# Performance work log

Measured on AMD Instinct MI355X. Metric: run time of the kernel, lower is better.

Reference implementation:

```python
import jax, jax.numpy as jnp
import numpy as np
from jax import lax

B = 16
IMG = 384
P = 16
C = 3
DIM = 256
DEPTH = 6
HEADS = 4
DH = 64
INNER = HEADS * DH  # 256
MLP = 512
NC = 21
HP = IMG // P       # 24
N = HP * HP         # 576
PD = C * P * P      # 768
K = 16
SCALE = DH ** -0.5
NEG = -1e9


def _ln(x, g, b):
    mu = x.mean(-1, keepdims=True)
    var = ((x - mu) ** 2).mean(-1, keepdims=True)
    return (x - mu) / jnp.sqrt(var + 1e-5) * g + b


def _conv(x, w, b):
    y = lax.conv_general_dilated(x, w, (1, 1), 'SAME',
                                 dimension_numbers=('NCHW', 'OIHW', 'NCHW'))
    return y + b[None, :, None, None]


def _up2(x):
    b, c, h, w = x.shape
    return jax.image.resize(x, (b, c, 2 * h, 2 * w), 'bilinear')


def _attn(x, g, bt, qkv_w, out_w, out_b, alpha):
    xn = _ln(x, g, bt)
    qkv = xn @ qkv_w                              # [B,N,3*INNER]
    q, k, v = jnp.split(qkv, 3, axis=-1)
    def heads(t):
        return t.reshape(B, N, HEADS, DH).transpose(0, 2, 1, 3)  # b h n d
    q, k, v = heads(q), heads(k), heads(v)
    dots = jnp.einsum('bhid,bhjd->bhij', q, k) * SCALE           # [B,H,N,N]
    vals, idx = lax.top_k(dots, K)                               # [B,H,N,K]
    bi = jnp.arange(B)[:, None, None, None]
    hi = jnp.arange(HEADS)[None, :, None, None]
    ni = jnp.arange(N)[None, None, :, None]
    sparse = jnp.full(dots.shape, NEG, dots.dtype).at[bi, hi, ni, idx].set(vals)
    sparse_attn = jax.nn.softmax(sparse, axis=-1)
    global_attn = jax.nn.softmax(dots, axis=-1)
    a = jnp.clip(alpha, 0.0, 1.0)
    attn = (1 - a) * sparse_attn + a * global_attn
    out = jnp.einsum('bhij,bhjd->bhid', attn, v)                 # [B,H,N,DH]
    out = out.transpose(0, 2, 1, 3).reshape(B, N, INNER)
    return out @ out_w + out_b


def _forward(img, patch_w, patch_b, pos_emb,
             ln1_g, ln1_b, qkv_w, out_w, out_b, alpha,
             ln2_g, ln2_b, ff_w1, ff_b1, ff_w2, ff_b2,
             lnf_g, lnf_b,
             conv1_w, conv1_b, conv2_w, conv2_b, conv3_w, conv3_b):
    # patchify: b c (h p1) (w p2) -> b (h w) (p1 p2 c)
    x = img.reshape(B, C, HP, P, HP, P).transpose(0, 2, 4, 3, 5, 1).reshape(B, N, PD)
    x = x @ patch_w + patch_b + pos_emb
    for i in range(DEPTH):
        x = x + _attn(x, ln1_g[i], ln1_b[i], qkv_w[i], out_w[i], out_b[i], alpha[i])
        h = _ln(x, ln2_g[i], ln2_b[i])
        h = jax.nn.gelu(h @ ff_w1[i] + ff_b1[i], approximate=False)
        x = x + h @ ff_w2[i] + ff_b2[i]
    x = _ln(x, lnf_g, lnf_b)
    x = x.transpose(0, 2, 1).reshape(B, DIM, HP, HP)             # b d h w
    x = jax.nn.relu(_conv(x, conv1_w, conv1_b))
    x = _up2(x)
    x = jax.nn.relu(_conv(x, conv2_w, conv2_b))
    x = _up2(x)
    x = _conv(x, conv3_w, conv3_b)
    return jax.image.resize(x, (B, NC, IMG, IMG), 'bilinear')


def setup_inputs() -> dict:
    key = jax.random.key(0)
    ks = jax.random.split(key, 16)
    s = 0.02
    d = {
        'img': jax.random.normal(ks[0], (B, C, IMG, IMG), jnp.float32),
        'patch_w': jax.random.normal(ks[1], (PD, DIM)) * s,
        'patch_b': jnp.zeros((DIM,)),
        'pos_emb': jax.random.normal(ks[2], (1, N, DIM)) * s,
        'ln1_g': jnp.ones((DEPTH, DIM)), 'ln1_b': jnp.zeros((DEPTH, DIM)),
        'qkv_w': jax.random.normal(ks[3], (DEPTH, DIM, 3 * INNER)) * s,
        'out_w': jax.random.normal(ks[4], (DEPTH, INNER, DIM)) * s,
        'out_b': jnp.zeros((DEPTH, DIM)),
        'alpha': jnp.full((DEPTH,), 0.2),
        'ln2_g': jnp.ones((DEPTH, DIM)), 'ln2_b': jnp.zeros((DEPTH, DIM)),
        'ff_w1': jax.random.normal(ks[5], (DEPTH, DIM, MLP)) * s,
        'ff_b1': jnp.zeros((DEPTH, MLP)),
        'ff_w2': jax.random.normal(ks[6], (DEPTH, MLP, DIM)) * s,
        'ff_b2': jnp.zeros((DEPTH, DIM)),
        'lnf_g': jnp.ones((DIM,)), 'lnf_b': jnp.zeros((DIM,)),
        'conv1_w': jax.random.normal(ks[7], (DIM // 2, DIM, 3, 3)) * s,
        'conv1_b': jnp.zeros((DIM // 2,)),
        'conv2_w': jax.random.normal(ks[8], (DIM // 4, DIM // 2, 3, 3)) * s,
        'conv2_b': jnp.zeros((DIM // 4,)),
        'conv3_w': jax.random.normal(ks[9], (NC, DIM // 4, 1, 1)) * s,
        'conv3_b': jnp.zeros((NC,)),
    }
    return d


def reference(img, patch_w, patch_b, pos_emb,
              ln1_g, ln1_b, qkv_w, out_w, out_b, alpha,
              ln2_g, ln2_b, ff_w1, ff_b1, ff_w2, ff_b2,
              lnf_g, lnf_b,
              conv1_w, conv1_b, conv2_w, conv2_b, conv3_w, conv3_b):
    return _forward(img, patch_w, patch_b, pos_emb,
                    ln1_g, ln1_b, qkv_w, out_w, out_b, alpha,
                    ln2_g, ln2_b, ff_w1, ff_b1, ff_w2, ff_b2,
                    lnf_g, lnf_b,
                    conv1_w, conv1_b, conv2_w, conv2_b, conv3_w, conv3_b)
```

## Files before the change

### kernel.cpp

```cpp
#include <hip/hip_runtime.h>
#include <cfloat>
#include <cmath>

constexpr int NB    = 16;
constexpr int IMGSZ = 384;
constexpr int PSZ   = 16;
constexpr int NCH   = 3;
constexpr int DMODEL= 256;
constexpr int DEPTH = 6;
constexpr int NHEAD = 4;
constexpr int DHEAD = 64;
constexpr int DQKV  = 768;
constexpr int QKS   = 512;
constexpr int DMLP  = 512;
constexpr int NCLS  = 21;
constexpr int HPATCH= 24;
constexpr int NTOK  = 576;
constexpr int NPD   = 768;
constexpr int TOPK  = 16;
constexpr int NROWS = NB * NTOK;
constexpr int OUT_TOTAL = NB * NCLS * IMGSZ * IMGSZ;

constexpr int RPB    = 16;
constexpr int NBLK   = NTOK / RPB;
constexpr int CHUNK  = 64;
constexpr int NCHUNK = NTOK / CHUNK;
constexpr int SCP    = 577;

typedef __attribute__((ext_vector_type(8))) short bf16x8;
typedef __attribute__((ext_vector_type(4))) float f32x4;

__device__ __forceinline__ unsigned short f2bf(float f) {
    unsigned u = __builtin_bit_cast(unsigned, f);
    unsigned r = (u + 0x7FFFu + ((u >> 16) & 1u)) >> 16;
    return (unsigned short)r;
}
__device__ __forceinline__ float bf2f(unsigned short h) {
    unsigned u = ((unsigned)h) << 16;
    return __builtin_bit_cast(float, u);
}

__global__ __launch_bounds__(256) void k_castT(const float* __restrict__ src,
                                               unsigned short* __restrict__ dst,
                                               int K, int N) {
    int t = blockIdx.x * 256 + threadIdx.x;
    if (t >= K * N) return;
    size_t base = (size_t)blockIdx.y * K * N;
    int n = t / K, k = t - n * K;
    dst[base + t] = f2bf(src[base + (size_t)k * N + n]);
}

template <int IC>
__global__ __launch_bounds__(256) void k_castConv(const float* __restrict__ src,
                                                  unsigned short* __restrict__ dst,
                                                  int OC) {
    int t = blockIdx.x * 256 + threadIdx.x;
    if (t >= OC * 9 * IC) return;
    int oc = t / (9 * IC);
    int r = t - oc * 9 * IC;
    int tap = r / IC, ic = r - tap * IC;
    dst[t] = f2bf(src[((size_t)(oc * IC + ic)) * 9 + tap]);
}

__global__ __launch_bounds__(256) void k_patchify(const float* __restrict__ img,
                                                  unsigned short* __restrict__ A) {
    int t = blockIdx.x * 256 + threadIdx.x;
    if (t >= NROWS * NPD) return;
    int r  = t / NPD, pd = t - r * NPD;
    int b  = r / NTOK, n = r - b * NTOK;
    int hy = n / HPATCH, hx = n - hy * HPATCH;
    int c  = pd % NCH;  int q = pd / NCH;
    int p2 = q % PSZ;   int p1 = q / PSZ;
    A[t] = f2bf(img[(((size_t)(b * NCH + c)) * IMGSZ + hy * PSZ + p1) * IMGSZ + hx * PSZ + p2]);
}

template <int BM, int BN, int EPI, int CIN>
__global__ __launch_bounds__(256) void k_mm(
    const unsigned short* __restrict__ Abf,
    const unsigned short* __restrict__ Wt,
    const float* __restrict__ bias,
    float* __restrict__ outf,
    unsigned short* __restrict__ outb,
    unsigned short* __restrict__ outb2,
    unsigned short* __restrict__ vth,
    unsigned short* __restrict__ vtl,
    int M, int Nn, int K, int H, int Wd, int gxd, int gyd)
{
    constexpr int MF = BM / 32;
    constexpr int NF = BN / 32;
    constexpr bool GATHER = (CIN > 0);
    constexpr int AREP = BM * 4 / 256;
    constexpr int BREP = BN * 4 / 256;
    __shared__ __align__(16) short As[4][BM][8];
    __shared__ __align__(16) short Bs[4][BN][8];
    const int tid = threadIdx.x;
    const int p = blockIdx.x;
    const int xr = p & 7, xq = p >> 3;
    const int bm = (xr * (gyd >> 3) + xq / gxd) * BM;
    const int bn = (xq % gxd) * BN;
    const int lane = tid & 63, wid = tid >> 6;
    const int wm = wid >> 1, wn = wid & 1;
    const int l15 = lane & 15, lg = lane >> 4;

    int pb_[AREP], py_[AREP], px_[AREP];
    if (GATHER) {
        #pragma unroll
        for (int rep = 0; rep < AREP; ++rep) {
            int idx = rep * 256 + tid;
            int m = idx >> 2;
            int pix = bm + m;
            px_[rep] = pix % Wd;
            int r = pix / Wd;
            py_[rep] = r % H;
            pb_[rep] = r / H;
        }
    }

    f32x4 acc[MF][NF];
    #pragma unroll
    for (int i = 0; i < MF; ++i)
        #pragma unroll
        for (int j = 0; j < NF; ++j)
            acc[i][j] = (f32x4){0.f, 0.f, 0.f, 0.f};

    for (int k0 = 0; k0 < K; k0 += 32) {
        #pragma unroll
        for (int rep = 0; rep < AREP; ++rep) {
            int idx = rep * 256 + tid;
            int m = idx >> 2, kg = idx & 3;
            if (!GATHER) {
                *(bf16x8*)As[kg][m] =
                    *(const bf16x8*)(Abf + (size_t)(bm + m) * K + k0 + kg * 8);
            } else {
                int k = k0 + kg * 8;
                int tap = k / CIN;
                int ic = k - tap * CIN;
                int dy = tap / 3 - 1, dx = tap % 3 - 1;
                int yy = py_[rep] + dy, xx = px_[rep] + dx;
                bf16x8 v = (bf16x8){0, 0, 0, 0, 0, 0, 0, 0};
                if ((unsigned)yy < (unsigned)H && (unsigned)xx < (unsigned)Wd)
                    v = *(const bf16x8*)(Abf +
                        ((size_t)((pb_[rep] * H + yy) * Wd + xx)) * CIN + ic);
                *(bf16x8*)As[kg][m] = v;
            }
        }
        #pragma unroll
        for (int rep = 0; rep < BREP; ++rep) {
            int idx = rep * 256 + tid;
            int n = idx >> 2, kg = idx & 3;
            *(bf16x8*)Bs[kg][n] =
                *(const bf16x8*)(Wt + (size_t)(bn + n) * K + k0 + kg * 8);
        }
        __syncthreads();
        bf16x8 af[MF], bfv[NF];
        #pragma unroll
        for (int i = 0; i < MF; ++i)
            af[i] = *(const bf16x8*)As[lg][wm * (BM / 2) + i * 16 + l15];
        #pragma unroll
        for (int j = 0; j < NF; ++j)
            bfv[j] = *(const bf16x8*)Bs[lg][wn * (BN / 2) + j * 16 + l15];
        #pragma unroll
        for (int i = 0; i < MF; ++i)
            #pragma unroll
            for (int j = 0; j < NF; ++j)
                acc[i][j] = __builtin_amdgcn_mfma_f32_16x16x32_bf16(
                    af[i], bfv[j], acc[i][j], 0, 0, 0);
        __syncthreads();
    }

    if constexpr (EPI == 8) {
        #pragma unroll
        for (int i = 0; i < MF; ++i) {
            const int row0 = bm + wm * (BM / 2) + i * 16 + lg * 4;
            #pragma unroll
            for (int j = 0; j < NF; ++j) {
                const int col = bn + wn * (BN / 2) + j * 16 + l15;
                if (col < 512) {
                    #pragma unroll
                    for (int r = 0; r < 4; ++r) {
                        float v = acc[i][j][r];
                        unsigned short hi = f2bf(v);
                        outb[(size_t)(row0 + r) * QKS + col] = hi;
                        outb2[(size_t)(row0 + r) * QKS + col] = f2bf(v - bf2f(hi));
                    }
                } else {
                    const int d = col - 512, hh = d >> 6, dd = d & 63;
                    const int bb = row0 / NTOK, n = row0 % NTOK;
                    unsigned long long ph = 0ull, pl = 0ull;
                    #pragma unroll
                    for (int r = 0; r < 4; ++r) {
                        float v = acc[i][j][r];
                        unsigned short hi = f2bf(v);
                        unsigned short lo = f2bf(v - bf2f(hi));
                        ph |= (unsigned long long)hi << (16 * r);
                        pl |= (unsigned long long)lo << (16 * r);
                    }
                    const size_t off = (size_t)((bb * NHEAD + hh) * DHEAD + dd) * NTOK + n;
                    *(unsigned long long*)(vth + off) = ph;
                    *(unsigned long long*)(vtl + off) = pl;
                }
            }
        }
    } else {
        #pragma unroll
        for (int i = 0; i < MF; ++i) {
            const int row0 = bm + wm * (BM / 2) + i * 16 + lg * 4;
            #pragma unroll
            for (int j = 0; j < NF; ++j) {
                const int col = bn + wn * (BN / 2) + j * 16 + l15;
                #pragma unroll
                for (int r = 0; r < 4; ++r) {
                    const int rr = row0 + r;
                    float v = acc[i][j][r] + bias[col];
                    if (EPI == 2) v = 0.5f * v * (1.0f + erff(v * 0.70710678118f));
                    if (EPI == 4) v = fmaxf(v, 0.f);
                    outb[(size_t)rr * Nn + col] = f2bf(v);
                }
            }
        }
    }
}

template <int RES>
__global__ __launch_bounds__(256) void k_gemm_ln(
    const unsigned short* __restrict__ Abf,
    const unsigned short* __restrict__ Wt,
    const float* __restrict__ bias,
    const float* __restrict__ extra,
    const float* __restrict__ lng,
    const float* __restrict__ lnb,
    float* __restrict__ x,
    unsigned short* __restrict__ xn,
    int K, int gyd)
{
    constexpr int BM = 32;
    __shared__ __align__(16) short As[4][BM][8];
    __shared__ __align__(16) short Bs[4][256][8];
    __shared__ float redS[BM][4];
    __shared__ float redQ[BM][4];
    const int tid = threadIdx.x;
    const int p = blockIdx.x;
    const int xr = p & 7, xq = p >> 3;
    const int bm = (xr * (gyd >> 3) + xq) * BM;
    const int lane = tid & 63, wn = tid >> 6;
    const int l15 = lane & 15, lg = lane >> 4;

    f32x4 acc[2][4];
    #pragma unroll
    for (int i = 0; i < 2; ++i)
        #pragma unroll
        for (int j = 0; j < 4; ++j)
            acc[i][j] = (f32x4){0.f, 0.f, 0.f, 0.f};

    for (int k0 = 0; k0 < K; k0 += 32) {
        if (tid < BM * 4) {
            int m = tid >> 2, kg = tid & 3;
            *(bf16x8*)As[kg][m] = *(const bf16x8*)(Abf + (size_t)(bm + m) * K + k0 + kg * 8);
        }
        #pragma unroll
        for (int rep = 0; rep < 4; ++rep) {
            int idx = rep * 256 + tid;
            int n = idx >> 2, kg = idx & 3;
            *(bf16x8*)Bs[kg][n] = *(const bf16x8*)(Wt + (size_t)n * K + k0 + kg * 8);
        }
        __syncthreads();
        bf16x8 af[2], bfv[4];
        #pragma unroll
        for (int i = 0; i < 2; ++i)
            af[i] = *(const bf16x8*)As[lg][i * 16 + l15];
        #pragma unroll
        for (int j = 0; j < 4; ++j)
            bfv[j] = *(const bf16x8*)Bs[lg][wn * 64 + j * 16 + l15];
        #pragma unroll
        for (int i = 0; i < 2; ++i)
            #pragma unroll
            for (int j = 0; j < 4; ++j)
                acc[i][j] = __builtin_amdgcn_mfma_f32_16x16x32_bf16(
                    af[i], bfv[j], acc[i][j], 0, 0, 0);
        __syncthreads();
    }

    #pragma unroll
    for (int i = 0; i < 2; ++i) {
        #pragma unroll
        for (int j = 0; j < 4; ++j) {
            const int col = wn * 64 + j * 16 + l15;
            #pragma unroll
            for (int r = 0; r < 4; ++r) {
                const int rr = bm + i * 16 + lg * 4 + r;
                float v = acc[i][j][r] + bias[col];
                if (RES) v += x[(size_t)rr * DMODEL + col];
                else     v += extra[(size_t)(rr % NTOK) * DMODEL + col];
                x[(size_t)rr * DMODEL + col] = v;
                acc[i][j][r] = v;
            }
        }
    }
    float s[2][4];
    #pragma unroll
    for (int i = 0; i < 2; ++i)
        #pragma unroll
        for (int r = 0; r < 4; ++r)
            s[i][r] = ((acc[i][0][r] + acc[i][1][r]) + acc[i][2][r]) + acc[i][3][r];
    #pragma unroll
    for (int off = 1; off < 16; off <<= 1)
        #pragma unroll
        for (int i = 0; i < 2; ++i)
            #pragma unroll
            for (int r = 0; r < 4; ++r)
                s[i][r] += __shfl_xor(s[i][r], off);
    if (l15 == 0)
        #pragma unroll
        for (int i = 0; i < 2; ++i)
            #pragma unroll
            for (int r = 0; r < 4; ++r)
                redS[i * 16 + lg * 4 + r][wn] = s[i][r];
    __syncthreads();
    float mu[2][4];
    #pragma unroll
    for (int i = 0; i < 2; ++i)
        #pragma unroll
        for (int r = 0; r < 4; ++r) {
            const float* q = redS[i * 16 + lg * 4 + r];
            mu[i][r] = (((q[0] + q[1]) + q[2]) + q[3]) * (1.0f / DMODEL);
        }
    float qq[2][4];
    #pragma unroll
    for (int i = 0; i < 2; ++i)
        #pragma unroll
        for (int r = 0; r < 4; ++r) {
            float d0 = acc[i][0][r] - mu[i][r], d1 = acc[i][1][r] - mu[i][r];
            float d2 = acc[i][2][r] - mu[i][r], d3 = acc[i][3][r] - mu[i][r];
            qq[i][r] = ((d0 * d0 + d1 * d1) + d2 * d2) + d3 * d3;
        }
    #pragma unroll
    for (int off = 1; off < 16; off <<= 1)
        #pragma unroll
        for (int i = 0; i < 2; ++i)
            #pragma unroll
            for (int r = 0; r < 4; ++r)
                qq[i][r] += __shfl_xor(qq[i][r], off);
    if (l15 == 0)
        #pragma unroll
        for (int i = 0; i < 2; ++i)
            #pragma unroll
            for (int r = 0; r < 4; ++r)
                redQ[i * 16 + lg * 4 + r][wn] = qq[i][r];
    __syncthreads();
    #pragma unroll
    for (int i = 0; i < 2; ++i) {
        #pragma unroll
        for (int r = 0; r < 4; ++r) {
            const float* q = redQ[i * 16 + lg * 4 + r];
            float var = (((q[0] + q[1]) + q[2]) + q[3]) * (1.0f / DMODEL);
            float rstd = rsqrtf(var + 1e-5f);
            const int rr = bm + i * 16 + lg * 4 + r;
            #pragma unroll
            for (int j = 0; j < 4; ++j) {
                const int col = wn * 64 + j * 16 + l15;
                float o = (acc[i][j][r] - mu[i][r]) * rstd * lng[col] + lnb[col];
                xn[(size_t)rr * DMODEL + col] = f2bf(o);
            }
        }
    }
}

struct KF { bf16x8 h0, h1, l0, l1; };
__device__ __forceinline__ KF ldkf(const unsigned short* __restrict__ hi,
                                   const unsigned short* __restrict__ lo,
                                   size_t off) {
    KF f;
    f.h0 = *(const bf16x8*)(hi + off);
    f.h1 = *(const bf16x8*)(hi + off + 32);
    f.l0 = *(const bf16x8*)(lo + off);
    f.l1 = *(const bf16x8*)(lo + off + 32);
    return f;
}

__global__ __launch_bounds__(512, 8) void k_attn(
    const unsigned short* __restrict__ qhi,
    const unsigned short* __restrict__ qlo,
    const unsigned short* __restrict__ vthi,
    const unsigned short* __restrict__ vtlo,
    const float* __restrict__ alpha_l,
    unsigned short* __restrict__ ao) {
    __shared__ __align__(16) unsigned char ub[16 * SCP * 4];
    float* scp = (float*)ub;
    short* pj  = (short*)ub;
    float* red = (float*)(ub + 16384);

    const int tid = threadIdx.x;
    const int lane = tid & 63;
    const int w = tid >> 6;
    const int par = w >> 2;
    const int ct = w & 3;
    const int l15 = lane & 15, lg = lane >> 4;
    const int xr = blockIdx.x & 7, xq = blockIdx.x >> 3;
    const int g = xr + 8 * (xq / NBLK);
    const int b = g >> 2, h = g & 3;
    const int i0 = (xq % NBLK) * RPB;

    bf16x8 aqh0, aqh1, aql0, aql1;
    {
        const size_t qoff = (size_t)(b * NTOK + i0 + l15) * QKS + h * DHEAD + lg * 8;
        aqh0 = *(const bf16x8*)(qhi + qoff);
        aqh1 = *(const bf16x8*)(qhi + qoff + 32);
        aql0 = *(const bf16x8*)(qlo + qoff);
        aql1 = *(const bf16x8*)(qlo + qoff + 32);
    }

    const size_t kRow = (size_t)(b * NTOK + ct * 16 + l15) * QKS + DMODEL + h * DHEAD + lg * 8;
    for (int c = par; c < NCHUNK; c += 2) {
        KF kc = ldkf(qhi, qlo, kRow + (size_t)c * CHUNK * QKS);
        f32x4 sD = (f32x4){0.f, 0.f, 0.f, 0.f};
        sD = __builtin_amdgcn_mfma_f32_16x16x32_bf16(aqh0, kc.h0, sD, 0, 0, 0);
        sD = __builtin_amdgcn_mfma_f32_16x16x32_bf16(aqh0, kc.l0, sD, 0, 0, 0);
        sD = __builtin_amdgcn_mfma_f32_16x16x32_bf16(aql0, kc.h0, sD, 0, 0, 0);
        sD = __builtin_amdgcn_mfma_f32_16x16x32_bf16(aqh1, kc.h1, sD, 0, 0, 0);
        sD = __builtin_amdgcn_mfma_f32_16x16x32_bf16(aqh1, kc.l1, sD, 0, 0, 0);
        sD = __builtin_amdgcn_mfma_f32_16x16x32_bf16(aql1, kc.h1, sD, 0, 0, 0);
        const int col = c * CHUNK + ct * 16 + l15;
        #pragma unroll
        for (int r = 0; r < 4; ++r)
            scp[(lg * 4 + r) * SCP + col] = sD[r] * 0.125f;
    }
    __syncthreads();

    float o_[2][9];
    const int r0 = 2 * w;
    #pragma unroll
    for (int rr = 0; rr < 2; ++rr)
        #pragma unroll
        for (int t = 0; t < 9; ++t)
            o_[rr][t] = scp[(r0 + rr) * SCP + t * 64 + lane];
    __syncthreads();

    unsigned msk[2] = {0u, 0u};
    float M_[2];
    for (int k = 0; k < TOPK; ++k) {
        float lm[2];
        #pragma unroll
        for (int rr = 0; rr < 2; ++rr) {
            float m0 = -FLT_MAX;
            #pragma unroll
            for (int t = 0; t < 9; ++t) {
                float v = ((msk[rr] >> t) & 1u) ? -FLT_MAX : o_[rr][t];
                m0 = fmaxf(m0, v);
            }
            lm[rr] = m0;
        }
        #pragma unroll
        for (int off = 1; off < 64; off <<= 1) {
            #pragma unroll
            for (int rr = 0; rr < 2; ++rr)
                lm[rr] = fmaxf(lm[rr], __shfl_xor(lm[rr], off));
        }
        if (k == 0) {
            #pragma unroll
            for (int rr = 0; rr < 2; ++rr) M_[rr] = lm[rr];
        }
        #pragma unroll
        for (int rr = 0; rr < 2; ++rr) {
            int js = -1;
            #pragma unroll
            for (int t = 0; t < 9; ++t) {
                if (js < 0) {
                    unsigned long long bal =
                        __ballot((((msk[rr] >> t) & 1u) == 0u) && (o_[rr][t] == lm[rr]));
                    if (bal) js = t * 64 + (int)__builtin_ctzll(bal);
                }
            }
            if ((js & 63) == lane) msk[rr] |= 1u << (js >> 6);
        }
    }

    const float al = fminf(fmaxf(alpha_l[0], 0.f), 1.f);
    float gs[2], ss[2];
    #pragma unroll
    for (int rr = 0; rr < 2; ++rr) {
        float g_ = 0.f, s_ = 0.f;
        #pragma unroll
        for (int t = 0; t < 9; ++t) {
            float e = __expf(o_[rr][t] - M_[rr]);
            g_ += e;
            if ((msk[rr] >> t) & 1u) s_ += e;
        }
        gs[rr] = g_; ss[rr] = s_;
    }
    #pragma unroll
    for (int off = 1; off < 64; off <<= 1) {
        #pragma unroll
        for (int rr = 0; rr < 2; ++rr) {
            gs[rr] += __shfl_xor(gs[rr], off);
            ss[rr] += __shfl_xor(ss[rr], off);
        }
    }
    float ca[2], cs[2];
    #pragma unroll
    for (int rr = 0; rr < 2; ++rr) {
        ca[rr] = al / gs[rr];
        cs[rr] = (1.f - al) / ss[rr];
    }

    const size_t vRow = (size_t)((b * NHEAD + h) * DHEAD + ct * 16 + l15) * NTOK + lg * 8;
    f32x4 acc = (f32x4){0.f, 0.f, 0.f, 0.f};
    for (int c = 0; c < NCHUNK; ++c) {
        short* pb = pj + (c & 1) * (2 * 16 * 72);
        #pragma unroll
        for (int rr = 0; rr < 2; ++rr) {
            float e = __expf(o_[rr][c] - M_[rr]);
            float wv = e * (ca[rr] + (((msk[rr] >> c) & 1u) ? cs[rr] : 0.f));
            unsigned short hi = f2bf(wv);
            pb[(r0 + rr) * 72 + lane] = (short)hi;
            pb[16 * 72 + (r0 + rr) * 72 + lane] = (short)f2bf(wv - bf2f(hi));
        }
        __syncthreads();
        if ((c & 1) == par) {
            KF vc = ldkf(vthi, vtlo, vRow + (size_t)c * CHUNK);
            const short* pr = pb + l15 * 72 + lg * 8;
            bf16x8 ah0 = *(const bf16x8*)(pr);
            bf16x8 ah1 = *(const bf16x8*)(pr + 32);
            bf16x8 al0 = *(const bf16x8*)(pr + 16 * 72);
            bf16x8 al1 = *(const bf16x8*)(pr + 16 * 72 + 32);
            acc = __builtin_amdgcn_mfma_f32_16x16x32_bf16(ah0, vc.h0, acc, 0, 0, 0);
            acc = __builtin_amdgcn_mfma_f32_16x16x32_bf16(ah0, vc.l0, acc, 0, 0, 0);
            acc = __builtin_amdgcn_mfma_f32_16x16x32_bf16(al0, vc.h0, acc, 0, 0, 0);
            acc = __builtin_amdgcn_mfma_f32_16x16x32_bf16(ah1, vc.h1, acc, 0, 0, 0);
            acc = __builtin_amdgcn_mfma_f32_16x16x32_bf16(ah1, vc.l1, acc, 0, 0, 0);
            acc = __builtin_amdgcn_mfma_f32_16x16x32_bf16(al1, vc.h1, acc, 0, 0, 0);
        }
    }
    if (par == 1) {
        #pragma unroll
        for (int r = 0; r < 4; ++r)
            red[(ct * 16 + l15) * 17 + lg * 4 + r] = acc[r];
    }
    __syncthreads();
    if (par == 0) {
        const int qrow = i0 + lg * 4;
        const int dcol = h * DHEAD + ct * 16 + l15;
        #pragma unroll
        for (int r = 0; r < 4; ++r) {
            float v = acc[r] + red[(ct * 16 + l15) * 17 + lg * 4 + r];
            ao[(size_t)(b * NTOK + qrow + r) * DMODEL + dcol] = f2bf(v);
        }
    }
}

__device__ __forceinline__ void bilin_axis(float sF, int H, int& i0, int& i1, float& f) {
    float fl = floorf(sF);
    f = sF - fl;
    int lo = (int)fl;
    i0 = lo < 0 ? 0 : (lo > H - 1 ? H - 1 : lo);
    int hi = lo + 1;
    i1 = hi < 0 ? 0 : (hi > H - 1 ? H - 1 : hi);
}

__global__ __launch_bounds__(256) void k_up2n(const unsigned short* __restrict__ in,
                                              unsigned short* __restrict__ outp,
                                              int Hin, int C) {
    const int Ho = 2 * Hin;
    const int CG = C / 8;
    const int total = NB * Ho * Ho * CG;
    int t = blockIdx.x * 256 + threadIdx.x;
    if (t >= total) return;
    int cg = t % CG; int r = t / CG;
    int x = r % Ho; r /= Ho;
    int y = r % Ho; int b = r / Ho;
    int i0, i1, j0, j1; float fy, fx;
    bilin_axis(0.5f * y - 0.25f, Hin, i0, i1, fy);
    bilin_axis(0.5f * x - 0.25f, Hin, j0, j1, fx);
    const unsigned short* base = in + (size_t)b * Hin * Hin * C + cg * 8;
    const bf16x8 p00 = *(const bf16x8*)(base + (size_t)(i0 * Hin + j0) * C);
    const bf16x8 p01 = *(const bf16x8*)(base + (size_t)(i0 * Hin + j1) * C);
    const bf16x8 p10 = *(const bf16x8*)(base + (size_t)(i1 * Hin + j0) * C);
    const bf16x8 p11 = *(const bf16x8*)(base + (size_t)(i1 * Hin + j1) * C);
    bf16x8 o;
    #pragma unroll
    for (int e = 0; e < 8; ++e) {
        float v = (1.f - fy) * ((1.f - fx) * bf2f((unsigned short)p00[e]) + fx * bf2f((unsigned short)p01[e]))
                + fy        * ((1.f - fx) * bf2f((unsigned short)p10[e]) + fx * bf2f((unsigned short)p11[e]));
        o[e] = (short)f2bf(v);
    }
    *(bf16x8*)(outp + (size_t)t * 8) = o;
}

__global__ __launch_bounds__(256) void k_conv3n(const unsigned short* __restrict__ in,
                                                const float* __restrict__ w,
                                                const float* __restrict__ bias,
                                                float* __restrict__ outp) {
    __shared__ float ws_[NCLS * 64];
    for (int i = threadIdx.x; i < NCLS * 64; i += 256) ws_[i] = w[i];
    __syncthreads();
    int t = blockIdx.x * 256 + threadIdx.x;
    if (t >= NB * 9216) return;
    int pix = t % 9216, b = t / 9216;
    float xv[64];
    const unsigned short* p = in + (size_t)t * 64;
    #pragma unroll
    for (int c = 0; c < 8; ++c) {
        bf16x8 v = *(const bf16x8*)(p + c * 8);
        #pragma unroll
        for (int e = 0; e < 8; ++e) xv[c * 8 + e] = bf2f((unsigned short)v[e]);
    }
    float* op = outp + (size_t)b * NCLS * 9216 + pix;
    #pragma unroll
    for (int o = 0; o < NCLS; ++o) {
        float acc = bias[o];
        #pragma unroll
        for (int ic = 0; ic < 64; ++ic) acc += ws_[o * 64 + ic] * xv[ic];
        op[(size_t)o * 9216] = acc;
    }
}

__global__ __launch_bounds__(256) void k_resize4(const float* __restrict__ in,
                                                 float* __restrict__ outp) {
    int t = blockIdx.x * 256 + threadIdx.x;
    if (t >= OUT_TOTAL) return;
    int x = t % IMGSZ; int r = t / IMGSZ; int y = r % IMGSZ; int bc = r / IMGSZ;
    int i0, i1, j0, j1; float fy, fx;
    bilin_axis(0.25f * y - 0.375f, 96, i0, i1, fy);
    bilin_axis(0.25f * x - 0.375f, 96, j0, j1, fx);
    const float* p = in + (size_t)bc * 9216;
    outp[t] = (1.f - fy) * ((1.f - fx) * p[i0 * 96 + j0] + fx * p[i0 * 96 + j1])
            + fy        * ((1.f - fx) * p[i1 * 96 + j0] + fx * p[i1 * 96 + j1]);
}

extern "C" void kernel_launch(void* const* d_in, const int* in_sizes, int n_in,
                              void* d_out, int out_size, void* d_ws, size_t ws_size,
                              hipStream_t stream) {
    const float* img     = (const float*)d_in[0];
    const float* patch_w = (const float*)d_in[1];
    const float* patch_b = (const float*)d_in[2];
    const float* pos_emb = (const float*)d_in[3];
    const float* ln1_g   = (const float*)d_in[4];
    const float* ln1_b   = (const float*)d_in[5];
    const float* qkv_w   = (const float*)d_in[6];
    const float* out_w   = (const float*)d_in[7];
    const float* out_b   = (const float*)d_in[8];
    const float* alpha   = (const float*)d_in[9];
    const float* ln2_g   = (const float*)d_in[10];
    const float* ln2_b   = (const float*)d_in[11];
    const float* ff_w1   = (const float*)d_in[12];
    const float* ff_b1   = (const float*)d_in[13];
    const float* ff_w2   = (const float*)d_in[14];
    const float* ff_b2   = (const float*)d_in[15];
    const float* lnf_g   = (const float*)d_in[16];
    const float* lnf_b   = (const float*)d_in[17];
    const float* conv1_w = (const float*)d_in[18];
    const float* conv1_b = (const float*)d_in[19];
    const float* conv2_w = (const float*)d_in[20];
    const float* conv2_b = (const float*)d_in[21];
    const float* conv3_w = (const float*)d_in[22];
    const float* conv3_b = (const float*)d_in[23];

    float* x = (float*)d_ws;
    unsigned short* qkv_hi = (unsigned short*)(x + (size_t)NROWS * DMODEL);
    unsigned short* qkv_lo = qkv_hi + (size_t)NROWS * QKS;
    unsigned short* xn_bf  = qkv_lo + (size_t)NROWS * QKS;
    unsigned short* ao_bf  = xn_bf + (size_t)NROWS * DMODEL;
    unsigned short* h_bf   = ao_bf + (size_t)NROWS * DMODEL;
    unsigned short* pA     = h_bf + (size_t)NROWS * DMLP;
    unsigned short* wts    = pA + (size_t)NROWS * NPD;
    unsigned short* pwt  = wts;
    unsigned short* qwt  = pwt  + 768 * 256;
    unsigned short* owt  = qwt  + 6 * 768 * 256;
    unsigned short* f1wt = owt  + 6 * 256 * 256;
    unsigned short* f2wt = f1wt + 6 * 256 * 512;
    unsigned short* c1wt = f2wt + 6 * 512 * 256;
    unsigned short* c2wt = c1wt + 128 * 9 * 256;
    unsigned short* vthi = c2wt + 64 * 9 * 128;
    unsigned short* vtlo = vthi + (size_t)64 * 64 * NTOK;
    unsigned short* c1n = ao_bf;
    unsigned short* u1n = h_bf;
    unsigned short* c2n = xn_bf;
    unsigned short* u2n = qkv_hi;
    float* c3 = (float*)pA;

    k_castT<<<dim3(768, 1), 256, 0, stream>>>(patch_w, pwt, NPD, DMODEL);
    k_castT<<<dim3(768, 6), 256, 0, stream>>>(qkv_w, qwt, DMODEL, DQKV);
    k_castT<<<dim3(256, 6), 256, 0, stream>>>(out_w, owt, DMODEL, DMODEL);
    k_castT<<<dim3(512, 6), 256, 0, stream>>>(ff_w1, f1wt, DMODEL, DMLP);
    k_castT<<<dim3(512, 6), 256, 0, stream>>>(ff_w2, f2wt, DMLP, DMODEL);
    k_castConv<256><<<1152, 256, 0, stream>>>(conv1_w, c1wt, 128);
    k_castConv<128><<<288, 256, 0, stream>>>(conv2_w, c2wt, 64);

    k_patchify<<<(NROWS * NPD + 255) / 256, 256, 0, stream>>>(img, pA);
    k_gemm_ln<0><<<288, 256, 0, stream>>>(
        pA, pwt, patch_b, pos_emb, ln1_g, ln1_b, x, xn_bf, NPD, 288);

    for (int l = 0; l < DEPTH; ++l) {
        k_mm<128, 128, 8, 0><<<6 * 72, 256, 0, stream>>>(
            xn_bf, qwt + (size_t)l * DQKV * DMODEL, nullptr,
            nullptr, qkv_hi, qkv_lo, vthi, vtlo,
            NROWS, DQKV, DMODEL, 0, 0, 6, 72);
        k_attn<<<NBLK * NHEAD * NB, 512, 0, stream>>>(
            qkv_hi, qkv_lo, vthi, vtlo, alpha + l, ao_bf);
        k_gemm_ln<1><<<288, 256, 0, stream>>>(
            ao_bf, owt + (size_t)l * DMODEL * DMODEL, out_b + l * DMODEL, nullptr,
            ln2_g + l * DMODEL, ln2_b + l * DMODEL, x, xn_bf, DMODEL, 288);
        k_mm<128, 128, 2, 0><<<4 * 72, 256, 0, stream>>>(
            xn_bf, f1wt + (size_t)l * DMLP * DMODEL, ff_b1 + l * DMLP,
            nullptr, h_bf, nullptr, nullptr, nullptr,
            NROWS, DMLP, DMODEL, 0, 0, 4, 72);
        const float* ng = (l + 1 < DEPTH) ? (ln1_g + (l + 1) * DMODEL) : lnf_g;
        const float* nb = (l + 1 < DEPTH) ? (ln1_b + (l + 1) * DMODEL) : lnf_b;
        k_gemm_ln<1><<<288, 256, 0, stream>>>(
            h_bf, f2wt + (size_t)l * DMODEL * DMLP, ff_b2 + l * DMODEL, nullptr,
            ng, nb, x, xn_bf, DMLP, 288);
    }

    k_mm<64, 128, 4, 256><<<1 * 144, 256, 0, stream>>>(
        xn_bf, c1wt, conv1_b, nullptr, c1n, nullptr, nullptr, nullptr,
        NROWS, 128, 9 * 256, 24, 24, 1, 144);
    k_up2n<<<(NB * 48 * 48 * 16 + 255) / 256, 256, 0, stream>>>(c1n, u1n, 24, 128);
    k_mm<128, 64, 4, 128><<<1 * 288, 256, 0, stream>>>(
        u1n, c2wt, conv2_b, nullptr, c2n, nullptr, nullptr, nullptr,
        NB * 48 * 48, 64, 9 * 128, 48, 48, 1, 288);
    k_up2n<<<(NB * 96 * 96 * 8 + 255) / 256, 256, 0, stream>>>(c2n, u2n, 48, 64);
    k_conv3n<<<(NB * 9216 + 255) / 256, 256, 0, stream>>>(u2n, conv3_w, conv3_b, c3);
    k_resize4<<<(OUT_TOTAL + 255) / 256, 256, 0, stream>>>(c3, (float*)d_out);
}
```

Before: 1.306 ms.

## Write all attention weights to LDS once and prefetch V chunks in PV loop

The per-chunk loop, which wrote probability tiles to a double-buffered LDS area and synchronized on every chunk, is replaced by one pass that writes all 9 chunks of hi/lo bf16 weights into a padded LDS buffer, followed by a single barrier. The PV MFMA loop then runs with no barriers, and each wave-half software-prefetches its next V chunk from global memory. This removes eight block-wide barriers and overlaps V loads with MFMA work. In exchange it uses a larger LDS footprint and more registers, which may reduce occupancy.

```diff
diff --git a/kernel.cpp b/kernel.cpp
--- a/kernel.cpp
+++ b/kernel.cpp
@@ -26,6 +26,7 @@
 constexpr int CHUNK  = 64;
 constexpr int NCHUNK = NTOK / CHUNK;
 constexpr int SCP    = 577;
+constexpr int PPS    = 584;
 
 typedef __attribute__((ext_vector_type(8))) short bf16x8;
 typedef __attribute__((ext_vector_type(4))) float f32x4;
@@ -384,10 +385,10 @@
     const unsigned short* __restrict__ vtlo,
     const float* __restrict__ alpha_l,
     unsigned short* __restrict__ ao) {
-    __shared__ __align__(16) unsigned char ub[16 * SCP * 4];
+    __shared__ __align__(16) unsigned char ub[2 * RPB * PPS * 2];
     float* scp = (float*)ub;
-    short* pj  = (short*)ub;
-    float* red = (float*)(ub + 16384);
+    short* php = (short*)ub;
+    float* red = (float*)ub;
 
     const int tid = threadIdx.x;
     const int lane = tid & 63;
@@ -502,34 +503,41 @@
         cs[rr] = (1.f - al) / ss[rr];
     }
 
+    #pragma unroll
+    for (int rr = 0; rr < 2; ++rr) {
+        const int row = r0 + rr;
+        #pragma unroll
+        for (int t = 0; t < 9; ++t) {
+            float e = __expf(o_[rr][t] - M_[rr]);
+            float wv = e * (ca[rr] + (((msk[rr] >> t) & 1u) ? cs[rr] : 0.f));
+            unsigned short hi = f2bf(wv);
+            php[row * PPS + t * 64 + lane] = (short)hi;
+            php[RPB * PPS + row * PPS + t * 64 + lane] = (short)f2bf(wv - bf2f(hi));
+        }
+    }
+    __syncthreads();
+
     const size_t vRow = (size_t)((b * NHEAD + h) * DHEAD + ct * 16 + l15) * NTOK + lg * 8;
     f32x4 acc = (f32x4){0.f, 0.f, 0.f, 0.f};
-    for (int c = 0; c < NCHUNK; ++c) {
-        short* pb = pj + (c & 1) * (2 * 16 * 72);
-        #pragma unroll
-        for (int rr = 0; rr < 2; ++rr) {
-            float e = __expf(o_[rr][c] - M_[rr]);
-            float wv = e * (ca[rr] + (((msk[rr] >> c) & 1u) ? cs[rr] : 0.f));
-            unsigned short hi = f2bf(wv);
-            pb[(r0 + rr) * 72 + lane] = (short)hi;
-            pb[16 * 72 + (r0 + rr) * 72 + lane] = (short)f2bf(wv - bf2f(hi));
-        }
-        __syncthreads();
-        if ((c & 1) == par) {
-            KF vc = ldkf(vthi, vtlo, vRow + (size_t)c * CHUNK);
-            const short* pr = pb + l15 * 72 + lg * 8;
-            bf16x8 ah0 = *(const bf16x8*)(pr);
-            bf16x8 ah1 = *(const bf16x8*)(pr + 32);
-            bf16x8 al0 = *(const bf16x8*)(pr + 16 * 72);
-            bf16x8 al1 = *(const bf16x8*)(pr + 16 * 72 + 32);
-            acc = __builtin_amdgcn_mfma_f32_16x16x32_bf16(ah0, vc.h0, acc, 0, 0, 0);
-            acc = __builtin_amdgcn_mfma_f32_16x16x32_bf16(ah0, vc.l0, acc, 0, 0, 0);
-            acc = __builtin_amdgcn_mfma_f32_16x16x32_bf16(al0, vc.h0, acc, 0, 0, 0);
-            acc = __builtin_amdgcn_mfma_f32_16x16x32_bf16(ah1, vc.h1, acc, 0, 0, 0);
-            acc = __builtin_amdgcn_mfma_f32_16x16x32_bf16(ah1, vc.l1, acc, 0, 0, 0);
-            acc = __builtin_amdgcn_mfma_f32_16x16x32_bf16(al1, vc.h1, acc, 0, 0, 0);
-        }
-    }
+    KF vc = ldkf(vthi, vtlo, vRow + (size_t)par * CHUNK);
+    for (int c = par; c < NCHUNK; c += 2) {
+        KF vn;
+        if (c + 2 < NCHUNK)
+            vn = ldkf(vthi, vtlo, vRow + (size_t)(c + 2) * CHUNK);
+        const short* pr = php + l15 * PPS + c * 64 + lg * 8;
+        bf16x8 ah0 = *(const bf16x8*)(pr);
+        bf16x8 ah1 = *(const bf16x8*)(pr + 32);
+        bf16x8 al0 = *(const bf16x8*)(pr + RPB * PPS);
+        bf16x8 al1 = *(const bf16x8*)(pr + RPB * PPS + 32);
+        acc = __builtin_amdgcn_mfma_f32_16x16x32_bf16(ah0, vc.h0, acc, 0, 0, 0);
+        acc = __builtin_amdgcn_mfma_f32_16x16x32_bf16(ah0, vc.l0, acc, 0, 0, 0);
+        acc = __builtin_amdgcn_mfma_f32_16x16x32_bf16(al0, vc.h0, acc, 0, 0, 0);
+        acc = __builtin_amdgcn_mfma_f32_16x16x32_bf16(ah1, vc.h1, acc, 0, 0, 0);
+        acc = __builtin_amdgcn_mfma_f32_16x16x32_bf16(ah1, vc.l1, acc, 0, 0, 0);
+        acc = __builtin_amdgcn_mfma_f32_16x16x32_bf16(al1, vc.h1, acc, 0, 0, 0);
+        if (c + 2 < NCHUNK) vc = vn;
+    }
+    __syncthreads();
     if (par == 1) {
         #pragma unroll
         for (int r = 0; r < 4; ++r)
```

Measured after the change: 1.293 ms. No clear change (-1.0%).
